# Kernel optimization log

Hardware: AMD Instinct MI355X
Metric: run time of the kernel (lower is better)

Reference implementation:

```python
import jax, jax.numpy as jnp
import numpy as np

B, P, C, NY, NX, CMAP = 4, 48000, 64, 496, 432, 16

def setup_inputs() -> dict:
    key = jax.random.key(0)
    k1, k2, k3 = jax.random.split(key, 3)
    voxel_features = jax.random.normal(k1, (P, C), dtype=jnp.float32)
    # Unique (batch, y, x) cells so scatter-set semantics are deterministic
    # (torch's canvas[:, indices] = voxels is order-dependent on duplicates).
    flat = jax.random.permutation(k2, B * NY * NX)[:P]
    b = flat // (NY * NX)
    rem = flat % (NY * NX)
    y = rem // NX
    x = rem % NX
    coords = jnp.stack([b, jnp.zeros_like(b), y, x], axis=1).astype(jnp.int32)
    map_fm = jax.random.normal(k3, (B, NX, NY, CMAP), dtype=jnp.float32)
    return {"voxel_features": voxel_features, "coords": coords,
            "batch_size": B, "map_fm": map_fm}

def reference(voxel_features, coords, batch_size, map_fm):
    ny, nx = NY, NX
    n_ch = voxel_features.shape[1]
    # Fused global index: batch * (ny*nx) + y * nx + x  -> one scatter, no batch loop
    gidx = (coords[:, 0].astype(jnp.int32) * (ny * nx)
            + coords[:, 2].astype(jnp.int32) * nx
            + coords[:, 3].astype(jnp.int32))
    canvas = jnp.zeros((batch_size * ny * nx, n_ch), dtype=voxel_features.dtype)
    canvas = canvas.at[gidx].set(voxel_features)
    # [B*ny*nx, C] -> [B, C, ny, nx]
    canvas = canvas.reshape(batch_size, ny, nx, n_ch).transpose(0, 3, 1, 2)
    if map_fm is not None:
        if map_fm.ndim == 5:
            map_fm = jnp.squeeze(map_fm, 3)
        map_fm = jnp.transpose(map_fm, (0, 3, 2, 1))  # [B, nx, ny, Cm] -> [B, Cm, ny, nx]
        canvas = jnp.concatenate([canvas, map_fm], axis=1)
    return canvas
```

## Files before the change

### kernel.cpp

```cpp
#include <hip/hip_runtime.h>
#include <stdint.h>
#include <stddef.h>

typedef __attribute__((ext_vector_type(4))) float f32x4;
typedef __attribute__((ext_vector_type(4))) int   i32x4;

constexpr int B = 4, P = 48000, C = 64, NY = 496, NX = 432, CMAP = 16;
constexpr int CT  = C + CMAP;
constexpr int X4  = NX / 4;
constexpr int CQ  = C / 4;
constexpr int GV2 = B * CQ * NY * X4;
constexpr int NBV = GV2 / 256;
constexpr int XH  = NX / 2;
constexpr int XH4 = XH / 4;
constexpr int NBM = B * NY * 2;

__global__ void scatter_inv_kernel(const int* __restrict__ coords,
                                   int* __restrict__ inv) {
    int p = blockIdx.x * blockDim.x + threadIdx.x;
    if (p >= P) return;
    const int4 cd = ((const int4*)coords)[p];
    inv[(cd.x * NY + cd.z) * NX + cd.w] = p;
}

__global__ void __launch_bounds__(256) fused_fill_kernel(
        const float* __restrict__ vox, const float* __restrict__ map,
        const int* __restrict__ inv, float* __restrict__ out) {
    __shared__ __align__(16) float m_s[CMAP][XH];

    const int blk = blockIdx.x;
    const int tid = threadIdx.x;

    if (blk < NBM) {
        const int half = blk & 1;
        const int by   = blk >> 1;
        const int b    = by / NY;
        const int y    = by - b * NY;
        const int x0   = half * XH;

        const f32x4* map4 = (const f32x4*)map;
        for (int i = tid; i < XH * 4; i += 256) {
            int xh = i >> 2, q = i & 3;
            f32x4 mv = map4[((size_t)(b * NX + x0 + xh) * NY + y) * 4 + q];
            m_s[q * 4 + 0][xh] = mv.x;
            m_s[q * 4 + 1][xh] = mv.y;
            m_s[q * 4 + 2][xh] = mv.z;
            m_s[q * 4 + 3][xh] = mv.w;
        }
        __syncthreads();

        const size_t out_base = ((size_t)b * CT + C) * NY * NX
                              + (size_t)y * NX + x0;
        for (int idx = tid; idx < CMAP * XH4; idx += 256) {
            int cm = idx / XH4;
            int x4 = idx - cm * XH4;
            f32x4 v = *(const f32x4*)&m_s[cm][x4 * 4];
            __builtin_nontemporal_store(v,
                (f32x4*)(out + out_base + (size_t)cm * (NY * NX) + x4 * 4));
        }
    } else {
        int g = (blk - NBM) * 256 + tid;
        int x4   = g % X4;
        int rest = g / X4;
        int y   = rest % NY;
        int bcq = rest / NY;
        int cq  = bcq & (CQ - 1);
        int b   = bcq >> 4;
        int c0  = cq * 4;

        i32x4 p4 = ((const i32x4*)inv)[(b * NY + y) * X4 + x4];

        f32x4 r0 = (f32x4)0.f, r1 = (f32x4)0.f, r2 = (f32x4)0.f, r3 = (f32x4)0.f;
        if ((p4.x & p4.y & p4.z & p4.w) >= 0) {
            const f32x4* vox4 = (const f32x4*)vox;
            if (p4.x >= 0) r0 = vox4[(size_t)p4.x * CQ + cq];
            if (p4.y >= 0) r1 = vox4[(size_t)p4.y * CQ + cq];
            if (p4.z >= 0) r2 = vox4[(size_t)p4.z * CQ + cq];
            if (p4.w >= 0) r3 = vox4[(size_t)p4.w * CQ + cq];
        }

        float* ob = out + (((size_t)b * CT + c0) * NY + y) * NX + x4 * 4;
        const size_t PL = (size_t)NY * NX;
        f32x4 s;
        s.x = r0.x; s.y = r1.x; s.z = r2.x; s.w = r3.x;
        __builtin_nontemporal_store(s, (f32x4*)(ob));
        s.x = r0.y; s.y = r1.y; s.z = r2.y; s.w = r3.y;
        __builtin_nontemporal_store(s, (f32x4*)(ob + PL));
        s.x = r0.z; s.y = r1.z; s.z = r2.z; s.w = r3.z;
        __builtin_nontemporal_store(s, (f32x4*)(ob + 2 * PL));
        s.x = r0.w; s.y = r1.w; s.z = r2.w; s.w = r3.w;
        __builtin_nontemporal_store(s, (f32x4*)(ob + 3 * PL));
    }
}

__global__ void zero_vox_region_kernel(float* __restrict__ out) {
    int g = blockIdx.x * 256 + threadIdx.x;
    if (g >= B * C * NY * X4) return;
    int x4   = g % X4;
    int rest = g / X4;
    int y  = rest % NY;
    int bc = rest / NY;
    int c  = bc & (C - 1);
    int b  = bc >> 6;
    *(f32x4*)(out + (((size_t)b * CT + c) * NY + y) * NX + x4 * 4) = (f32x4)0.f;
}

__global__ void scatter_direct_kernel(const float* __restrict__ vox,
                                      const int* __restrict__ coords,
                                      float* __restrict__ out) {
    int p = blockIdx.x;
    int c = threadIdx.x;
    const int4 cd = ((const int4*)coords)[p];
    out[(((size_t)cd.x * CT + c) * NY + cd.z) * NX + cd.w] = vox[(size_t)p * C + c];
}

__global__ void map_only_kernel(const float* __restrict__ map,
                                float* __restrict__ out) {
    int g = blockIdx.x * 256 + threadIdx.x;
    if (g >= B * CMAP * NY * NX) return;
    int x    = g % NX;
    int rest = g / NX;
    int y  = rest % NY;
    int bc = rest / NY;
    int cm = bc & (CMAP - 1);
    int b  = bc >> 4;
    out[((size_t)b * CT + C + cm) * NY * NX + (size_t)y * NX + x] =
        map[((size_t)(b * NX + x) * NY + y) * CMAP + cm];
}

extern "C" void kernel_launch(void* const* d_in, const int* in_sizes, int n_in,
                              void* d_out, int out_size, void* d_ws, size_t ws_size,
                              hipStream_t stream) {
    const float* vox    = (const float*)d_in[0];
    const int*   coords = (const int*)d_in[1];
    const float* map    = (const float*)d_in[3];
    float* out = (float*)d_out;

    const size_t inv_bytes = (size_t)B * NY * NX * sizeof(int);
    int* inv = (ws_size >= inv_bytes) ? (int*)d_ws : nullptr;

    if (inv) {
        (void)hipMemsetAsync(inv, 0xFF, inv_bytes, stream);
        scatter_inv_kernel<<<(P + 255) / 256, 256, 0, stream>>>(coords, inv);
        fused_fill_kernel<<<NBM + NBV, 256, 0, stream>>>(vox, map, inv, out);
    } else {
        zero_vox_region_kernel<<<(B * C * NY * X4 + 255) / 256, 256, 0, stream>>>(out);
        scatter_direct_kernel<<<P, 64, 0, stream>>>(vox, coords, out);
        map_only_kernel<<<(B * CMAP * NY * NX + 255) / 256, 256, 0, stream>>>(map, out);
    }
}
```

Measured before the change: 331.3 us.

## Split fused fill into dense zero fill, sparse voxel write, and map transpose

Replaces the single fused fill kernel with three kernels. The first is a contiguous nontemporal zero fill of the voxel channel region. The second is a voxel kernel that exits early for quads with no occupied cells and writes only occupied ones. The third is a standalone map transpose kernel. The aim is to stop running the gather and transposed-store path for the mostly empty canvas, at the cost of writing occupied quads twice and paying two extra kernel launches.

```diff
diff --git a/kernel.cpp b/kernel.cpp
--- a/kernel.cpp
+++ b/kernel.cpp
@@ -14,6 +14,9 @@
 constexpr int XH  = NX / 2;
 constexpr int XH4 = XH / 4;
 constexpr int NBM = B * NY * 2;
+constexpr size_t PL = (size_t)NY * NX;
+constexpr int ZB  = (C * (int)PL * 4) / 16384;
+constexpr int NBZ = B * ZB;
 
 __global__ void scatter_inv_kernel(const int* __restrict__ coords,
                                    int* __restrict__ inv) {
@@ -23,73 +26,81 @@
     inv[(cd.x * NY + cd.z) * NX + cd.w] = p;
 }
 
-__global__ void __launch_bounds__(256) fused_fill_kernel(
-        const float* __restrict__ vox, const float* __restrict__ map,
-        const int* __restrict__ inv, float* __restrict__ out) {
+__global__ void __launch_bounds__(256) zero_vox4_kernel(float* __restrict__ out) {
+    const int blk = blockIdx.x;
+    const int b   = blk / ZB;
+    const int rb  = blk - b * ZB;
+    float* base = out + (size_t)b * CT * PL + (size_t)rb * 4096
+                      + (size_t)threadIdx.x * 4;
+    #pragma unroll
+    for (int k = 0; k < 4; ++k)
+        __builtin_nontemporal_store((f32x4)0.f, (f32x4*)(base + k * 1024));
+}
+
+__global__ void __launch_bounds__(256) vox_sparse_kernel(
+        const float* __restrict__ vox, const int* __restrict__ inv,
+        float* __restrict__ out) {
+    int g = blockIdx.x * 256 + threadIdx.x;
+    int x4   = g % X4;
+    int rest = g / X4;
+    int y   = rest % NY;
+    int bcq = rest / NY;
+    int cq  = bcq & (CQ - 1);
+    int b   = bcq >> 4;
+    int c0  = cq * 4;
+
+    i32x4 p4 = ((const i32x4*)inv)[(b * NY + y) * X4 + x4];
+    if ((p4.x & p4.y & p4.z & p4.w) < 0) return;
+
+    f32x4 r0 = (f32x4)0.f, r1 = (f32x4)0.f, r2 = (f32x4)0.f, r3 = (f32x4)0.f;
+    const f32x4* vox4 = (const f32x4*)vox;
+    if (p4.x >= 0) r0 = vox4[(size_t)p4.x * CQ + cq];
+    if (p4.y >= 0) r1 = vox4[(size_t)p4.y * CQ + cq];
+    if (p4.z >= 0) r2 = vox4[(size_t)p4.z * CQ + cq];
+    if (p4.w >= 0) r3 = vox4[(size_t)p4.w * CQ + cq];
+
+    float* ob = out + (((size_t)b * CT + c0) * NY + y) * NX + x4 * 4;
+    f32x4 s;
+    s.x = r0.x; s.y = r1.x; s.z = r2.x; s.w = r3.x;
+    __builtin_nontemporal_store(s, (f32x4*)(ob));
+    s.x = r0.y; s.y = r1.y; s.z = r2.y; s.w = r3.y;
+    __builtin_nontemporal_store(s, (f32x4*)(ob + PL));
+    s.x = r0.z; s.y = r1.z; s.z = r2.z; s.w = r3.z;
+    __builtin_nontemporal_store(s, (f32x4*)(ob + 2 * PL));
+    s.x = r0.w; s.y = r1.w; s.z = r2.w; s.w = r3.w;
+    __builtin_nontemporal_store(s, (f32x4*)(ob + 3 * PL));
+}
+
+__global__ void __launch_bounds__(256) map_half_kernel(
+        const float* __restrict__ map, float* __restrict__ out) {
     __shared__ __align__(16) float m_s[CMAP][XH];
 
     const int blk = blockIdx.x;
     const int tid = threadIdx.x;
+    const int half = blk & 1;
+    const int by   = blk >> 1;
+    const int b    = by / NY;
+    const int y    = by - b * NY;
+    const int x0   = half * XH;
 
-    if (blk < NBM) {
-        const int half = blk & 1;
-        const int by   = blk >> 1;
-        const int b    = by / NY;
-        const int y    = by - b * NY;
-        const int x0   = half * XH;
+    const f32x4* map4 = (const f32x4*)map;
+    for (int i = tid; i < XH * 4; i += 256) {
+        int xh = i >> 2, q = i & 3;
+        f32x4 mv = map4[((size_t)(b * NX + x0 + xh) * NY + y) * 4 + q];
+        m_s[q * 4 + 0][xh] = mv.x;
+        m_s[q * 4 + 1][xh] = mv.y;
+        m_s[q * 4 + 2][xh] = mv.z;
+        m_s[q * 4 + 3][xh] = mv.w;
+    }
+    __syncthreads();
 
-        const f32x4* map4 = (const f32x4*)map;
-        for (int i = tid; i < XH * 4; i += 256) {
-            int xh = i >> 2, q = i & 3;
-            f32x4 mv = map4[((size_t)(b * NX + x0 + xh) * NY + y) * 4 + q];
-            m_s[q * 4 + 0][xh] = mv.x;
-            m_s[q * 4 + 1][xh] = mv.y;
-            m_s[q * 4 + 2][xh] = mv.z;
-            m_s[q * 4 + 3][xh] = mv.w;
-        }
-        __syncthreads();
-
-        const size_t out_base = ((size_t)b * CT + C) * NY * NX
-                              + (size_t)y * NX + x0;
-        for (int idx = tid; idx < CMAP * XH4; idx += 256) {
-            int cm = idx / XH4;
-            int x4 = idx - cm * XH4;
-            f32x4 v = *(const f32x4*)&m_s[cm][x4 * 4];
-            __builtin_nontemporal_store(v,
-                (f32x4*)(out + out_base + (size_t)cm * (NY * NX) + x4 * 4));
-        }
-    } else {
-        int g = (blk - NBM) * 256 + tid;
-        int x4   = g % X4;
-        int rest = g / X4;
-        int y   = rest % NY;
-        int bcq = rest / NY;
-        int cq  = bcq & (CQ - 1);
-        int b   = bcq >> 4;
-        int c0  = cq * 4;
-
-        i32x4 p4 = ((const i32x4*)inv)[(b * NY + y) * X4 + x4];
-
-        f32x4 r0 = (f32x4)0.f, r1 = (f32x4)0.f, r2 = (f32x4)0.f, r3 = (f32x4)0.f;
-        if ((p4.x & p4.y & p4.z & p4.w) >= 0) {
-            const f32x4* vox4 = (const f32x4*)vox;
-            if (p4.x >= 0) r0 = vox4[(size_t)p4.x * CQ + cq];
-            if (p4.y >= 0) r1 = vox4[(size_t)p4.y * CQ + cq];
-            if (p4.z >= 0) r2 = vox4[(size_t)p4.z * CQ + cq];
-            if (p4.w >= 0) r3 = vox4[(size_t)p4.w * CQ + cq];
-        }
-
-        float* ob = out + (((size_t)b * CT + c0) * NY + y) * NX + x4 * 4;
-        const size_t PL = (size_t)NY * NX;
-        f32x4 s;
-        s.x = r0.x; s.y = r1.x; s.z = r2.x; s.w = r3.x;
-        __builtin_nontemporal_store(s, (f32x4*)(ob));
-        s.x = r0.y; s.y = r1.y; s.z = r2.y; s.w = r3.y;
-        __builtin_nontemporal_store(s, (f32x4*)(ob + PL));
-        s.x = r0.z; s.y = r1.z; s.z = r2.z; s.w = r3.z;
-        __builtin_nontemporal_store(s, (f32x4*)(ob + 2 * PL));
-        s.x = r0.w; s.y = r1.w; s.z = r2.w; s.w = r3.w;
-        __builtin_nontemporal_store(s, (f32x4*)(ob + 3 * PL));
+    const size_t out_base = ((size_t)b * CT + C) * PL + (size_t)y * NX + x0;
+    for (int idx = tid; idx < CMAP * XH4; idx += 256) {
+        int cm = idx / XH4;
+        int x4 = idx - cm * XH4;
+        f32x4 v = *(const f32x4*)&m_s[cm][x4 * 4];
+        __builtin_nontemporal_store(v,
+            (f32x4*)(out + out_base + (size_t)cm * PL + x4 * 4));
     }
 }
 
@@ -124,7 +135,7 @@
     int bc = rest / NY;
     int cm = bc & (CMAP - 1);
     int b  = bc >> 4;
-    out[((size_t)b * CT + C + cm) * NY * NX + (size_t)y * NX + x] =
+    out[((size_t)b * CT + C + cm) * PL + (size_t)y * NX + x] =
         map[((size_t)(b * NX + x) * NY + y) * CMAP + cm];
 }
 
@@ -142,7 +153,9 @@
     if (inv) {
         (void)hipMemsetAsync(inv, 0xFF, inv_bytes, stream);
         scatter_inv_kernel<<<(P + 255) / 256, 256, 0, stream>>>(coords, inv);
-        fused_fill_kernel<<<NBM + NBV, 256, 0, stream>>>(vox, map, inv, out);
+        zero_vox4_kernel<<<NBZ, 256, 0, stream>>>(out);
+        vox_sparse_kernel<<<NBV, 256, 0, stream>>>(vox, inv, out);
+        map_half_kernel<<<NBM, 256, 0, stream>>>(map, out);
     } else {
         zero_vox_region_kernel<<<(B * C * NY * X4 + 255) / 256, 256, 0, stream>>>(out);
         scatter_direct_kernel<<<P, 64, 0, stream>>>(vox, coords, out);
```

After: 393.2 us. 1.19x slower.

## Split fused fill into separate voxel and map-transpose kernels with 3D grids

Applied to the files above, without the earlier changes.

Splits the single fused kernel into two launches. The voxel fill now uses a 3D grid with 108 active lanes per half-block covering two rows, which removes the div/mod index math but leaves some threads idle. The map transpose kernel tiles two y rows per block with padded shared memory and unrolled loops. The cost is an extra kernel launch and a lost chance to overlap the two regions within one grid.

```diff
diff --git a/kernel.cpp b/kernel.cpp
--- a/kernel.cpp
+++ b/kernel.cpp
@@ -9,11 +9,9 @@
 constexpr int CT  = C + CMAP;
 constexpr int X4  = NX / 4;
 constexpr int CQ  = C / 4;
-constexpr int GV2 = B * CQ * NY * X4;
-constexpr int NBV = GV2 / 256;
 constexpr int XH  = NX / 2;
 constexpr int XH4 = XH / 4;
-constexpr int NBM = B * NY * 2;
+constexpr size_t PL = (size_t)NY * NX;
 
 __global__ void scatter_inv_kernel(const int* __restrict__ coords,
                                    int* __restrict__ inv) {
@@ -23,73 +21,78 @@
     inv[(cd.x * NY + cd.z) * NX + cd.w] = p;
 }
 
-__global__ void __launch_bounds__(256) fused_fill_kernel(
-        const float* __restrict__ vox, const float* __restrict__ map,
-        const int* __restrict__ inv, float* __restrict__ out) {
-    __shared__ __align__(16) float m_s[CMAP][XH];
+__global__ void __launch_bounds__(256) vox_fill_kernel(
+        const float* __restrict__ vox, const int* __restrict__ inv,
+        float* __restrict__ out) {
+    const int x4  = threadIdx.x & 127;
+    if (x4 >= X4) return;
+    const int y   = (blockIdx.y << 1) | (threadIdx.x >> 7);
+    const int bcq = blockIdx.z;
+    const int cq  = bcq & (CQ - 1);
+    const int b   = bcq >> 4;
+    const int c0  = cq * 4;
 
-    const int blk = blockIdx.x;
-    const int tid = threadIdx.x;
+    i32x4 p4 = ((const i32x4*)inv)[(b * NY + y) * X4 + x4];
 
-    if (blk < NBM) {
-        const int half = blk & 1;
-        const int by   = blk >> 1;
-        const int b    = by / NY;
-        const int y    = by - b * NY;
-        const int x0   = half * XH;
+    f32x4 r0 = (f32x4)0.f, r1 = (f32x4)0.f, r2 = (f32x4)0.f, r3 = (f32x4)0.f;
+    if ((p4.x & p4.y & p4.z & p4.w) >= 0) {
+        const f32x4* vox4 = (const f32x4*)vox;
+        if (p4.x >= 0) r0 = vox4[(size_t)p4.x * CQ + cq];
+        if (p4.y >= 0) r1 = vox4[(size_t)p4.y * CQ + cq];
+        if (p4.z >= 0) r2 = vox4[(size_t)p4.z * CQ + cq];
+        if (p4.w >= 0) r3 = vox4[(size_t)p4.w * CQ + cq];
+    }
 
-        const f32x4* map4 = (const f32x4*)map;
-        for (int i = tid; i < XH * 4; i += 256) {
-            int xh = i >> 2, q = i & 3;
-            f32x4 mv = map4[((size_t)(b * NX + x0 + xh) * NY + y) * 4 + q];
-            m_s[q * 4 + 0][xh] = mv.x;
-            m_s[q * 4 + 1][xh] = mv.y;
-            m_s[q * 4 + 2][xh] = mv.z;
-            m_s[q * 4 + 3][xh] = mv.w;
+    float* ob = out + (((size_t)b * CT + c0) * NY + y) * NX + x4 * 4;
+    f32x4 s;
+    s.x = r0.x; s.y = r1.x; s.z = r2.x; s.w = r3.x;
+    __builtin_nontemporal_store(s, (f32x4*)(ob));
+    s.x = r0.y; s.y = r1.y; s.z = r2.y; s.w = r3.y;
+    __builtin_nontemporal_store(s, (f32x4*)(ob + PL));
+    s.x = r0.z; s.y = r1.z; s.z = r2.z; s.w = r3.z;
+    __builtin_nontemporal_store(s, (f32x4*)(ob + 2 * PL));
+    s.x = r0.w; s.y = r1.w; s.z = r2.w; s.w = r3.w;
+    __builtin_nontemporal_store(s, (f32x4*)(ob + 3 * PL));
+}
+
+__global__ void __launch_bounds__(256) map_tile_kernel(
+        const float* __restrict__ map, float* __restrict__ out) {
+    __shared__ __align__(16) float m_s[2][CMAP][XH + 4];
+
+    const int tid  = threadIdx.x;
+    const int half = blockIdx.x;
+    const int y0   = blockIdx.y << 1;
+    const int b    = blockIdx.z;
+    const int x0   = half * XH;
+
+    const f32x4* map4 = (const f32x4*)map;
+    #pragma unroll
+    for (int k = 0; k < 7; ++k) {
+        int idx = k * 256 + tid;
+        if (idx < XH * 8) {
+            int xh = idx >> 3, r = idx & 7, yy = r >> 2, q = r & 3;
+            f32x4 mv = map4[((size_t)(b * NX + x0 + xh) * NY + y0 + yy) * 4 + q];
+            m_s[yy][q * 4 + 0][xh] = mv.x;
+            m_s[yy][q * 4 + 1][xh] = mv.y;
+            m_s[yy][q * 4 + 2][xh] = mv.z;
+            m_s[yy][q * 4 + 3][xh] = mv.w;
         }
-        __syncthreads();
+    }
+    __syncthreads();
 
-        const size_t out_base = ((size_t)b * CT + C) * NY * NX
-                              + (size_t)y * NX + x0;
-        for (int idx = tid; idx < CMAP * XH4; idx += 256) {
-            int cm = idx / XH4;
-            int x4 = idx - cm * XH4;
-            f32x4 v = *(const f32x4*)&m_s[cm][x4 * 4];
+    const size_t out_base = ((size_t)b * CT + C) * PL + (size_t)y0 * NX + x0;
+    #pragma unroll
+    for (int k = 0; k < 8; ++k) {
+        int idx = k * 256 + tid;
+        int sl  = idx & 63;
+        int cmy = idx >> 6;
+        int cm  = cmy >> 1, yy = cmy & 1;
+        if (sl < XH4) {
+            f32x4 v = *(const f32x4*)&m_s[yy][cm][sl * 4];
             __builtin_nontemporal_store(v,
-                (f32x4*)(out + out_base + (size_t)cm * (NY * NX) + x4 * 4));
+                (f32x4*)(out + out_base + (size_t)cm * PL
+                             + (size_t)yy * NX + sl * 4));
         }
-    } else {
-        int g = (blk - NBM) * 256 + tid;
-        int x4   = g % X4;
-        int rest = g / X4;
-        int y   = rest % NY;
-        int bcq = rest / NY;
-        int cq  = bcq & (CQ - 1);
-        int b   = bcq >> 4;
-        int c0  = cq * 4;
-
-        i32x4 p4 = ((const i32x4*)inv)[(b * NY + y) * X4 + x4];
-
-        f32x4 r0 = (f32x4)0.f, r1 = (f32x4)0.f, r2 = (f32x4)0.f, r3 = (f32x4)0.f;
-        if ((p4.x & p4.y & p4.z & p4.w) >= 0) {
-            const f32x4* vox4 = (const f32x4*)vox;
-            if (p4.x >= 0) r0 = vox4[(size_t)p4.x * CQ + cq];
-            if (p4.y >= 0) r1 = vox4[(size_t)p4.y * CQ + cq];
-            if (p4.z >= 0) r2 = vox4[(size_t)p4.z * CQ + cq];
-            if (p4.w >= 0) r3 = vox4[(size_t)p4.w * CQ + cq];
-        }
-
-        float* ob = out + (((size_t)b * CT + c0) * NY + y) * NX + x4 * 4;
-        const size_t PL = (size_t)NY * NX;
-        f32x4 s;
-        s.x = r0.x; s.y = r1.x; s.z = r2.x; s.w = r3.x;
-        __builtin_nontemporal_store(s, (f32x4*)(ob));
-        s.x = r0.y; s.y = r1.y; s.z = r2.y; s.w = r3.y;
-        __builtin_nontemporal_store(s, (f32x4*)(ob + PL));
-        s.x = r0.z; s.y = r1.z; s.z = r2.z; s.w = r3.z;
-        __builtin_nontemporal_store(s, (f32x4*)(ob + 2 * PL));
-        s.x = r0.w; s.y = r1.w; s.z = r2.w; s.w = r3.w;
-        __builtin_nontemporal_store(s, (f32x4*)(ob + 3 * PL));
     }
 }
 
@@ -124,7 +127,7 @@
     int bc = rest / NY;
     int cm = bc & (CMAP - 1);
     int b  = bc >> 4;
-    out[((size_t)b * CT + C + cm) * NY * NX + (size_t)y * NX + x] =
+    out[((size_t)b * CT + C + cm) * PL + (size_t)y * NX + x] =
         map[((size_t)(b * NX + x) * NY + y) * CMAP + cm];
 }
 
@@ -142,7 +145,8 @@
     if (inv) {
         (void)hipMemsetAsync(inv, 0xFF, inv_bytes, stream);
         scatter_inv_kernel<<<(P + 255) / 256, 256, 0, stream>>>(coords, inv);
-        fused_fill_kernel<<<NBM + NBV, 256, 0, stream>>>(vox, map, inv, out);
+        vox_fill_kernel<<<dim3(1, NY / 2, B * CQ), 256, 0, stream>>>(vox, inv, out);
+        map_tile_kernel<<<dim3(2, NY / 2, B), 256, 0, stream>>>(map, out);
     } else {
         zero_vox_region_kernel<<<(B * C * NY * X4 + 255) / 256, 256, 0, stream>>>(out);
         scatter_direct_kernel<<<P, 64, 0, stream>>>(vox, coords, out);
```

After: 332.4 us. Within noise of the previous version (+0.3%).
